# Performance work log

Hardware: AMD Instinct MI355X
Metric: run time of the kernel (lower is better)

Reference implementation:

```python
import jax, jax.numpy as jnp
import numpy as np

BATCH = 8192
MAX_ATOMS = 512  # angles_max_length


def setup_inputs() -> dict:
    key = jax.random.key(0)
    k1, k2, k3 = jax.random.split(key, 3)
    inp = jax.random.normal(k1, (BATCH, 3 * MAX_ATOMS), dtype=jnp.float32)
    tgt = jax.random.normal(k2, (BATCH, 3 * MAX_ATOMS), dtype=jnp.float32)
    num_atoms = jax.random.randint(k3, (BATCH,), 0, MAX_ATOMS, dtype=jnp.int64)
    num_atoms = jnp.maximum(num_atoms, 16)  # avoid degenerate tiny structures
    return {"input": inp, "target": tgt, "num_atoms": num_atoms}


def _kabsch_rmsd(inp, tgt, num_atoms):
    B = inp.shape[0]
    N = inp.shape[1] // 3
    src = inp.reshape(B, N, 3)
    dst = tgt.reshape(B, N, 3)
    # mask out padding atoms
    mask = (jnp.arange(N)[None, :] < num_atoms[:, None])[..., None]  # [B,N,1]
    n = num_atoms.astype(inp.dtype)[:, None, None]                   # [B,1,1]
    src = jnp.where(mask, src, 0.0)
    dst = jnp.where(dst.dtype.type(0) == 0, jnp.where(mask, dst, 0.0), dst)
    # center on masked centroid, re-zero padding
    src_c = jnp.where(mask, src - jnp.sum(src, axis=1, keepdims=True) / n, 0.0)
    dst_c = jnp.where(mask, dst - jnp.sum(dst, axis=1, keepdims=True) / n, 0.0)
    # 3x3 correlation matrices
    R = jnp.einsum("bni,bnj->bij", src_c, dst_c)  # [B,3,3]
    U, S, Vt = jnp.linalg.svd(R)
    d = jnp.sign(jnp.linalg.det(U) * jnp.linalg.det(Vt))  # chirality correction
    trace_opt = S[:, 0] + S[:, 1] + d * S[:, 2]
    sq = jnp.sum(src_c * src_c, axis=(1, 2)) + jnp.sum(dst_c * dst_c, axis=(1, 2))
    na = num_atoms.astype(inp.dtype)
    msd = (sq - 2.0 * trace_opt) / na
    return jnp.sqrt(jnp.clip(msd, 0.0))


def reference(input, target, num_atoms):
    return _kabsch_rmsd(input, target, num_atoms)
```

## Files before the change

kernel.cpp:

```cpp
#include <hip/hip_runtime.h>
#include <math.h>

#define NATOMS 512
#define TPB 256
#define WPB 4
#define FPE (3 * NATOMS)
#define LDSF (2 * FPE)

__device__ __forceinline__ void async_copy16(const float* g, float* l) {
    __builtin_amdgcn_global_load_lds(
        (const __attribute__((address_space(1))) void*)g,
        (__attribute__((address_space(3))) void*)l,
        16, 0, 0);
}

template <int CTRL>
__device__ __forceinline__ float dpp_add(float x) {
    const int yi = __builtin_amdgcn_update_dpp(
        0, __float_as_int(x), CTRL, 0xf, 0xf, true);
    return x + __int_as_float(yi);
}
__device__ __forceinline__ float wave_sum63(float x) {
    x = dpp_add<0x111>(x);
    x = dpp_add<0x112>(x);
    x = dpp_add<0x114>(x);
    x = dpp_add<0x118>(x);
    x = dpp_add<0x142>(x);
    x = dpp_add<0x143>(x);
    return x;
}

__global__ __launch_bounds__(TPB) void kabsch_reduce_kernel(
    const float* __restrict__ inp,
    const float* __restrict__ tgt,
    const int* __restrict__ num_atoms,
    float* __restrict__ partial,
    int B)
{
    __shared__ float lds[WPB * LDSF];

    const int wave = threadIdx.x >> 6;
    const int lane = threadIdx.x & 63;
    const int b = blockIdx.x * WPB + wave;
    if (b >= B) return;

    const int na = num_atoms[b];
    const float* gs = inp + (size_t)b * FPE;
    const float* gd = tgt + (size_t)b * FPE;
    float* myLds = lds + wave * LDSF;

    #pragma unroll
    for (int i = 0; i < 6; ++i)
        async_copy16(gs + i * 256 + lane * 4, myLds + i * 256);
    #pragma unroll
    for (int i = 0; i < 6; ++i)
        async_copy16(gd + i * 256 + lane * 4, myLds + FPE + i * 256);

    __builtin_amdgcn_s_waitcnt(0x0f70);
    asm volatile("" ::: "memory");

    float v[16];
    #pragma unroll
    for (int i = 0; i < 16; ++i) v[i] = 0.f;

    #pragma unroll
    for (int k = 0; k < 8; ++k) {
        const int atom = 64 * k + lane;
        const int off = 3 * atom;
        const float m = (atom < na) ? 1.f : 0.f;
        const float sx = myLds[off]           * m;
        const float sy = myLds[off + 1]       * m;
        const float sz = myLds[off + 2]       * m;
        const float dx = myLds[FPE + off]     * m;
        const float dy = myLds[FPE + off + 1] * m;
        const float dz = myLds[FPE + off + 2] * m;
        v[0]  += sx * dx;  v[1]  += sx * dy;  v[2]  += sx * dz;
        v[3]  += sy * dx;  v[4]  += sy * dy;  v[5]  += sy * dz;
        v[6]  += sz * dx;  v[7]  += sz * dy;  v[8]  += sz * dz;
        v[9]  += sx;  v[10] += sy;  v[11] += sz;
        v[12] += dx;  v[13] += dy;  v[14] += dz;
        v[15] += sx * sx + sy * sy + sz * sz + dx * dx + dy * dy + dz * dz;
    }

    #pragma unroll
    for (int i = 0; i < 16; ++i) v[i] = wave_sum63(v[i]);

    if (lane == 63) {
        float4* p = (float4*)(partial + (size_t)b * 16);
        p[0] = make_float4(v[0],  v[1],  v[2],  v[3]);
        p[1] = make_float4(v[4],  v[5],  v[6],  v[7]);
        p[2] = make_float4(v[8],  v[9],  v[10], v[11]);
        p[3] = make_float4(v[12], v[13], v[14], v[15]);
    }
}

__global__ __launch_bounds__(TPB) void kabsch_epilogue_kernel(
    const float* __restrict__ partial,
    const int* __restrict__ num_atoms,
    float* __restrict__ out,
    int B)
{
    const int b = blockIdx.x * TPB + threadIdx.x;
    if (b >= B) return;

    const float4* p = (const float4*)(partial + (size_t)b * 16);
    const float4 r0 = p[0], r1 = p[1], r2 = p[2], r3 = p[3];
    float v[16] = { r0.x, r0.y, r0.z, r0.w,
                    r1.x, r1.y, r1.z, r1.w,
                    r2.x, r2.y, r2.z, r2.w,
                    r3.x, r3.y, r3.z, r3.w };

    const int na = num_atoms[b];
    const double n = (double)na;
    const double sx = (double)v[9],  sy = (double)v[10], sz = (double)v[11];
    const double tx = (double)v[12], ty = (double)v[13], tz = (double)v[14];

    double R[3][3];
    R[0][0] = (double)v[0] - sx * tx / n;
    R[0][1] = (double)v[1] - sx * ty / n;
    R[0][2] = (double)v[2] - sx * tz / n;
    R[1][0] = (double)v[3] - sy * tx / n;
    R[1][1] = (double)v[4] - sy * ty / n;
    R[1][2] = (double)v[5] - sy * tz / n;
    R[2][0] = (double)v[6] - sz * tx / n;
    R[2][1] = (double)v[7] - sz * ty / n;
    R[2][2] = (double)v[8] - sz * tz / n;

    const double sq = (double)v[15] - (sx * sx + sy * sy + sz * sz
                                     + tx * tx + ty * ty + tz * tz) / n;

    const double detR =
        R[0][0] * (R[1][1] * R[2][2] - R[1][2] * R[2][1])
      - R[0][1] * (R[1][0] * R[2][2] - R[1][2] * R[2][0])
      + R[0][2] * (R[1][0] * R[2][1] - R[1][1] * R[2][0]);

    double A00 = R[0][0]*R[0][0] + R[1][0]*R[1][0] + R[2][0]*R[2][0];
    double A11 = R[0][1]*R[0][1] + R[1][1]*R[1][1] + R[2][1]*R[2][1];
    double A22 = R[0][2]*R[0][2] + R[1][2]*R[1][2] + R[2][2]*R[2][2];
    double A01 = R[0][0]*R[0][1] + R[1][0]*R[1][1] + R[2][0]*R[2][1];
    double A02 = R[0][0]*R[0][2] + R[1][0]*R[1][2] + R[2][0]*R[2][2];
    double A12 = R[0][1]*R[0][2] + R[1][1]*R[1][2] + R[2][1]*R[2][2];

    double e0, e1, e2;
    const double p1 = A01*A01 + A02*A02 + A12*A12;
    if (p1 < 1e-30) {
        e0 = A00; e1 = A11; e2 = A22;
        double tmp;
        if (e0 < e1) { tmp = e0; e0 = e1; e1 = tmp; }
        if (e1 < e2) { tmp = e1; e1 = e2; e2 = tmp; }
        if (e0 < e1) { tmp = e0; e0 = e1; e1 = tmp; }
    } else {
        const double q  = (A00 + A11 + A22) / 3.0;
        const double b00 = A00 - q, b11 = A11 - q, b22 = A22 - q;
        const double p2 = b00*b00 + b11*b11 + b22*b22 + 2.0 * p1;
        const double pp = sqrt(p2 / 6.0);
        const double ip = 1.0 / pp;
        const double B00 = b00*ip, B11 = b11*ip, B22 = b22*ip;
        const double B01 = A01*ip, B02 = A02*ip, B12 = A12*ip;
        double r = 0.5 * (B00 * (B11 * B22 - B12 * B12)
                        - B01 * (B01 * B22 - B12 * B02)
                        + B02 * (B01 * B12 - B11 * B02));
        if (r < -1.0) r = -1.0;
        if (r >  1.0) r =  1.0;
        const double phi = acos(r) / 3.0;
        e0 = q + 2.0 * pp * cos(phi);
        e2 = q + 2.0 * pp * cos(phi + 2.0943951023931953);
        e1 = 3.0 * q - e0 - e2;
    }

    const double S0 = sqrt(e0 > 0.0 ? e0 : 0.0);
    const double S1 = sqrt(e1 > 0.0 ? e1 : 0.0);
    const double S2 = sqrt(e2 > 0.0 ? e2 : 0.0);
    const double dsgn = (detR > 0.0) ? 1.0 : ((detR < 0.0) ? -1.0 : 0.0);
    const double trace_opt = S0 + S1 + dsgn * S2;

    double msd = (sq - 2.0 * trace_opt) / n;
    if (msd < 0.0) msd = 0.0;
    out[b] = (float)sqrt(msd);
}

extern "C" void kernel_launch(void* const* d_in, const int* in_sizes, int n_in,
                              void* d_out, int out_size, void* d_ws, size_t ws_size,
                              hipStream_t stream) {
    const float* inp = (const float*)d_in[0];
    const float* tgt = (const float*)d_in[1];
    const int* num_atoms = (const int*)d_in[2];
    float* out = (float*)d_out;
    float* partial = (float*)d_ws;

    const int B = in_sizes[0] / FPE;
    const int blocks1 = (B + WPB - 1) / WPB;
    kabsch_reduce_kernel<<<blocks1, TPB, 0, stream>>>(inp, tgt, num_atoms, partial, B);
    const int blocks2 = (B + TPB - 1) / TPB;
    kabsch_epilogue_kernel<<<blocks2, TPB, 0, stream>>>(partial, num_atoms, out, B);
}
```

Measured before the change: 118.4 us.

## Skip padded atoms and load coordinates directly into registers with prefetch

Computes the number of 64-atom chunks actually needed from num_atoms and loops only over those, so padding atoms beyond the valid count are never read from global memory. The LDS staging via global_load_lds is replaced by direct per-lane float3 loads with a one-step software prefetch. This cuts memory traffic roughly in proportion to the unused padding, at the cost of a data-dependent loop, 12-byte strided loads, and less memory-level parallelism per wave.

```diff
diff --git a/kernel.cpp b/kernel.cpp
--- a/kernel.cpp
+++ b/kernel.cpp
@@ -5,14 +5,6 @@
 #define TPB 256
 #define WPB 4
 #define FPE (3 * NATOMS)
-#define LDSF (2 * FPE)
-
-__device__ __forceinline__ void async_copy16(const float* g, float* l) {
-    __builtin_amdgcn_global_load_lds(
-        (const __attribute__((address_space(1))) void*)g,
-        (__attribute__((address_space(3))) void*)l,
-        16, 0, 0);
-}
 
 template <int CTRL>
 __device__ __forceinline__ float dpp_add(float x) {
@@ -37,49 +29,43 @@
     float* __restrict__ partial,
     int B)
 {
-    __shared__ float lds[WPB * LDSF];
-
     const int wave = threadIdx.x >> 6;
     const int lane = threadIdx.x & 63;
     const int b = blockIdx.x * WPB + wave;
     if (b >= B) return;
 
     const int na = num_atoms[b];
-    const float* gs = inp + (size_t)b * FPE;
-    const float* gd = tgt + (size_t)b * FPE;
-    float* myLds = lds + wave * LDSF;
+    int kmax = (na + 63) >> 6;
+    if (kmax < 1) kmax = 1;
+    if (kmax > 8) kmax = 8;
 
-    #pragma unroll
-    for (int i = 0; i < 6; ++i)
-        async_copy16(gs + i * 256 + lane * 4, myLds + i * 256);
-    #pragma unroll
-    for (int i = 0; i < 6; ++i)
-        async_copy16(gd + i * 256 + lane * 4, myLds + FPE + i * 256);
-
-    __builtin_amdgcn_s_waitcnt(0x0f70);
-    asm volatile("" ::: "memory");
+    const float* gs = inp + (size_t)b * FPE + 3 * lane;
+    const float* gd = tgt + (size_t)b * FPE + 3 * lane;
 
     float v[16];
     #pragma unroll
     for (int i = 0; i < 16; ++i) v[i] = 0.f;
 
-    #pragma unroll
-    for (int k = 0; k < 8; ++k) {
-        const int atom = 64 * k + lane;
-        const int off = 3 * atom;
+    float3 scur = *(const float3*)gs;
+    float3 dcur = *(const float3*)gd;
+
+    for (int k = 0; k < kmax; ++k) {
+        float3 snxt = scur, dnxt = dcur;
+        if (k + 1 < kmax) {
+            snxt = *(const float3*)(gs + 192 * (k + 1));
+            dnxt = *(const float3*)(gd + 192 * (k + 1));
+        }
+        const int atom = (k << 6) + lane;
         const float m = (atom < na) ? 1.f : 0.f;
-        const float sx = myLds[off]           * m;
-        const float sy = myLds[off + 1]       * m;
-        const float sz = myLds[off + 2]       * m;
-        const float dx = myLds[FPE + off]     * m;
-        const float dy = myLds[FPE + off + 1] * m;
-        const float dz = myLds[FPE + off + 2] * m;
+        const float sx = scur.x * m, sy = scur.y * m, sz = scur.z * m;
+        const float dx = dcur.x * m, dy = dcur.y * m, dz = dcur.z * m;
         v[0]  += sx * dx;  v[1]  += sx * dy;  v[2]  += sx * dz;
         v[3]  += sy * dx;  v[4]  += sy * dy;  v[5]  += sy * dz;
         v[6]  += sz * dx;  v[7]  += sz * dy;  v[8]  += sz * dz;
         v[9]  += sx;  v[10] += sy;  v[11] += sz;
         v[12] += dx;  v[13] += dy;  v[14] += dz;
         v[15] += sx * sx + sy * sy + sz * sz + dx * dx + dy * dy + dz * dz;
+        scur = snxt; dcur = dnxt;
     }
 
     #pragma unroll
```

After: 114.3 us. 3.5% less time.
